# Kernel tuning notes

Measured on AMD Instinct MI355X. Metric: run time of the kernel, lower is better.

Reference implementation:

```python
import math
import jax, jax.numpy as jnp
import numpy as np

MAX_T = 300
B, T, V, D, H = 16, 256, 25, 128, 8


def _layernorm(x, g, b):
    m = x.mean(-1, keepdims=True)
    var = ((x - m) ** 2).mean(-1, keepdims=True)
    return (x - m) / jnp.sqrt(var + 1e-5) * g + b


def setup_inputs() -> dict:
    key = jax.random.key(0)
    ks = jax.random.split(key, 8)
    d = D // H
    init = lambda k, shape: jax.random.normal(k, shape, dtype=jnp.float32) * 0.02
    return dict(
        x=jax.random.normal(ks[0], (B, T, V, D), dtype=jnp.float32),
        ln1_g=jnp.ones((D,), jnp.float32), ln1_b=jnp.zeros((D,), jnp.float32),
        qkv_w=init(ks[1], (D, 3 * D)), qkv_b=jnp.zeros((3 * D,), jnp.float32),
        proj_w=init(ks[2], (D, D)), proj_b=jnp.zeros((D,), jnp.float32),
        logit_scale=jnp.full((H, 1, 1), math.log(math.sqrt(d)), dtype=jnp.float32),
        rel_pos_bias=init(ks[3], (H, 2 * MAX_T - 1)),
        ln2_g=jnp.ones((D,), jnp.float32), ln2_b=jnp.zeros((D,), jnp.float32),
        ffn_w1=init(ks[4], (D, 4 * D)), ffn_b1=jnp.zeros((4 * D,), jnp.float32),
        ffn_w2=init(ks[5], (4 * D, D)), ffn_b2=jnp.zeros((D,), jnp.float32),
    )


def reference(x, ln1_g, ln1_b, qkv_w, qkv_b, proj_w, proj_b, logit_scale,
              rel_pos_bias, ln2_g, ln2_b, ffn_w1, ffn_b1, ffn_w2, ffn_b2):
    b, t, v_, dm = x.shape
    h = logit_scale.shape[0]
    d = dm // h
    # (B, T, V, D) -> (B*V, T, D): attention runs over frames per joint
    xf = x.transpose(0, 2, 1, 3).reshape(b * v_, t, dm)
    res = xf
    xn = _layernorm(xf, ln1_g, ln1_b)
    qkv = (xn @ qkv_w + qkv_b).reshape(b * v_, t, 3, h, d).transpose(2, 0, 3, 1, 4)
    q, k, v = qkv[0], qkv[1], qkv[2]  # (BV, h, T, d)
    scale = jnp.exp(jnp.minimum(logit_scale, math.log(100.0)))  # (h,1,1)
    qn = q / jnp.maximum(jnp.linalg.norm(q, axis=-1, keepdims=True), 1e-12) * scale
    kn = k / jnp.maximum(jnp.linalg.norm(k, axis=-1, keepdims=True), 1e-12)
    # learned relative-position bias, gathered to (h, T, T)
    coords = jnp.arange(t)
    rel = coords[:, None] - coords[None, :] + (MAX_T - 1)
    bias = rel_pos_bias[:, rel]
    # SDPA applies its default 1/sqrt(head_dim) scale on top of logit_scale
    scores = jnp.einsum('bhtd,bhsd->bhts', qn, kn) / math.sqrt(d) + bias[None]
    attn = jax.nn.softmax(scores, axis=-1)
    out = jnp.einsum('bhts,bhsd->bhtd', attn, v)
    out = out.transpose(0, 2, 1, 3).reshape(b * v_, t, dm)
    xf = res + (out @ proj_w + proj_b)
    y = _layernorm(xf, ln2_g, ln2_b)
    y = jax.nn.gelu(y @ ffn_w1 + ffn_b1, approximate=False) @ ffn_w2 + ffn_b2
    xf = xf + y
    return xf.reshape(b, v_, t, dm).transpose(0, 2, 1, 3)
```

## Files before the change

### kernel.cpp

```cpp
#include <hip/hip_runtime.h>
#include <hip/hip_fp16.h>
#include <math.h>

#define B_   16
#define T_   256
#define V_   25
#define D_   128
#define H_   8
#define DH   16
#define BV_  (B_*V_)
#define MAXT 300
#define NREL (2*MAXT-1)

typedef __attribute__((ext_vector_type(8))) short short8;
typedef __attribute__((ext_vector_type(4))) float f32x4;
typedef __attribute__((ext_vector_type(4))) _Float16 half4;
typedef __attribute__((ext_vector_type(8))) _Float16 half8;

__device__ inline short f2bf(float f) {
  union { float f; unsigned u; } a; a.f = f;
  unsigned r = (a.u + 0x7FFF + ((a.u >> 16) & 1)) >> 16;
  return (short)r;
}

__device__ inline float gelu_fast(float u) {
  float s = u * fmaf(0.0713548162726f, u*u, 1.5957691216057f);
  return u * __builtin_amdgcn_rcpf(1.0f + __expf(-s));
}

__global__ __launch_bounds__(256) void k0_prep(
    const float* __restrict__ qkv_w, const float* __restrict__ pw,
    const float* __restrict__ w1,    const float* __restrict__ w2,
    short* __restrict__ qkv_wt, short* __restrict__ pwt,
    _Float16* __restrict__ w1t, _Float16* __restrict__ w2t)
{
  int i = blockIdx.x*256 + threadIdx.x;
  if (i < 384*128) { int n = i >> 7, k = i & 127; qkv_wt[i] = f2bf(qkv_w[k*384 + n]); }
  if (i < 128*128) { int n = i >> 7, k = i & 127; pwt[i]    = f2bf(pw[k*128 + n]); }
  if (i < 512*128) { int n = i >> 7, k = i & 127; w1t[i]    = (_Float16)w1[k*512 + n]; }
  if (i < 128*512) {
    int r = i & 3, lane = (i >> 2) & 63, hn = (i >> 8) & 31, ot = i >> 13;
    int k = hn*16 + (lane >> 4)*4 + r;
    int n = ot*16 + (lane & 15);
    w2t[i] = (_Float16)w2[k*128 + n];
  }
}

__global__ __launch_bounds__(256) void k1_ln_qkv(
    const float* __restrict__ x, const float* __restrict__ g1, const float* __restrict__ b1,
    const short* __restrict__ qkv_wt, const float* __restrict__ qkv_b,
    const float* __restrict__ logit_scale,
    _Float16* __restrict__ qb, _Float16* __restrict__ kb, _Float16* __restrict__ vt)
{
  __shared__ short xn[64][136];
  const int tid = threadIdx.x;
  const int bv  = blockIdx.x / (T_/64);
  const int t0  = (blockIdx.x % (T_/64)) * 64;
  const int b   = bv / V_, v = bv % V_;

  {
    const int j = tid & 15;
    float4 gA = *(const float4*)(g1 + j*8), gB = *(const float4*)(g1 + j*8 + 4);
    float4 bA = *(const float4*)(b1 + j*8), bB = *(const float4*)(b1 + j*8 + 4);
    float gg[8] = {gA.x,gA.y,gA.z,gA.w,gB.x,gB.y,gB.z,gB.w};
    float bb[8] = {bA.x,bA.y,bA.z,bA.w,bB.x,bB.y,bB.z,bB.w};
    for (int rep = 0; rep < 4; ++rep) {
      const int tok = rep*16 + (tid >> 4);
      const float* xp = x + (((size_t)b*T_ + (t0+tok))*V_ + v)*D_ + j*8;
      float4 a0 = *(const float4*)xp;
      float4 a1 = *(const float4*)(xp+4);
      float e[8] = {a0.x,a0.y,a0.z,a0.w,a1.x,a1.y,a1.z,a1.w};
      float s = 0.f;
      #pragma unroll
      for (int q = 0; q < 8; ++q) s += e[q];
      #pragma unroll
      for (int m = 1; m < 16; m <<= 1) s += __shfl_xor(s, m, 16);
      float mean = s * (1.0f/128.0f);
      float s2 = 0.f;
      #pragma unroll
      for (int q = 0; q < 8; ++q) { float d = e[q]-mean; s2 += d*d; }
      #pragma unroll
      for (int m = 1; m < 16; m <<= 1) s2 += __shfl_xor(s2, m, 16);
      float rstd = rsqrtf(s2*(1.0f/128.0f) + 1e-5f);
      short8 o;
      #pragma unroll
      for (int q = 0; q < 8; ++q) o[q] = f2bf((e[q]-mean)*rstd*gg[q] + bb[q]);
      *(short8*)&xn[tok][j*8] = o;
    }
  }
  __syncthreads();

  const int wave = tid >> 6, lane = tid & 63;
  const int col = lane & 15, quad = lane >> 4;
  short8 af[4][4];
  #pragma unroll
  for (int tt = 0; tt < 4; ++tt)
    #pragma unroll
    for (int kk = 0; kk < 4; ++kk)
      af[tt][kk] = *(const short8*)&xn[tt*16+col][kk*32 + quad*8];

  for (int it = 0; it < 6; ++it) {
    const int tile = wave*6 + it;
    const int n0 = tile*16;
    short8 bf[4];
    #pragma unroll
    for (int kk = 0; kk < 4; ++kk)
      bf[kk] = *(const short8*)(qkv_wt + (size_t)(n0+col)*128 + kk*32 + quad*8);
    f32x4 acc[4] = {{0.f,0.f,0.f,0.f},{0.f,0.f,0.f,0.f},{0.f,0.f,0.f,0.f},{0.f,0.f,0.f,0.f}};
    #pragma unroll
    for (int kk = 0; kk < 4; ++kk)
      #pragma unroll
      for (int tt = 0; tt < 4; ++tt)
        acc[tt] = __builtin_amdgcn_mfma_f32_16x16x32_bf16(af[tt][kk], bf[kk], acc[tt], 0, 0, 0);
    const float bias = qkv_b[n0+col];
    const int h = tile & 7;
    const size_t bh = (size_t)bv*H_ + h;
    if (tile < 16) {
      const float scale = (tile < 8)
        ? __expf(fminf(logit_scale[h], 4.605170185988091f)) * 0.25f : 1.0f;
      #pragma unroll
      for (int tt = 0; tt < 4; ++tt) {
        float val[4], inv[4];
        #pragma unroll
        for (int r = 0; r < 4; ++r) {
          val[r] = acc[tt][r] + bias;
          float s = val[r]*val[r];
          #pragma unroll
          for (int m = 1; m < 16; m <<= 1) s += __shfl_xor(s, m, 16);
          inv[r] = 1.0f / fmaxf(sqrtf(s), 1e-12f);
        }
        const size_t obase = (bh*T_ + (t0 + tt*16 + quad*4))*DH + col;
        if (tile < 8) {
          #pragma unroll
          for (int r = 0; r < 4; ++r) qb[obase + (size_t)r*DH] = (_Float16)(val[r]*inv[r]*scale);
        } else {
          #pragma unroll
          for (int r = 0; r < 4; ++r) kb[obase + (size_t)r*DH] = (_Float16)(val[r]*inv[r]);
        }
      }
    } else {
      #pragma unroll
      for (int tt = 0; tt < 4; ++tt) {
        half4 vh;
        #pragma unroll
        for (int r = 0; r < 4; ++r) vh[r] = (_Float16)(acc[tt][r] + bias);
        *(half4*)(vt + bh*4096 + (size_t)(t0/16 + tt)*256 + col*16 + quad*4) = vh;
      }
    }
  }
}

__global__ __launch_bounds__(256) void k2_attn(
    const float* __restrict__ rel_pos_bias,
    const _Float16* __restrict__ qb, const _Float16* __restrict__ kb,
    const _Float16* __restrict__ vt, float* __restrict__ xattn)
{
  __shared__ float bias_s[NREL + 1];
  const int tid = threadIdx.x;
  const int bh  = blockIdx.x;
  const int h   = bh & (H_-1);
  const int bv  = bh >> 3;
  for (int j = tid; j < NREL; j += 256) bias_s[j] = rel_pos_bias[h*NREL + j];
  __syncthreads();

  const int wave = tid >> 6, lane = tid & 63;
  const int nn = lane & 15, quad = lane >> 4;
  const size_t qkbase = (size_t)bh * (T_*DH);
  const size_t vbase  = (size_t)bh * 4096;

  half4 qf[4];
  #pragma unroll
  for (int tt = 0; tt < 4; ++tt)
    qf[tt] = *(const half4*)(qb + qkbase + (size_t)(wave*64 + tt*16 + nn)*DH + quad*4);

  f32x4 o[4];
  #pragma unroll
  for (int tt = 0; tt < 4; ++tt) o[tt] = (f32x4){0.f,0.f,0.f,0.f};
  float lsum[4] = {0.f,0.f,0.f,0.f};

  half4 kf = *(const half4*)(kb + qkbase + (size_t)nn*DH + quad*4);
  half4 vf = *(const half4*)(vt + vbase + (size_t)nn*16 + quad*4);

  for (int s16 = 0; s16 < 16; ++s16) {
    half4 kf_n, vf_n;
    if (s16 < 15) {
      kf_n = *(const half4*)(kb + qkbase + (size_t)((s16+1)*16 + nn)*DH + quad*4);
      vf_n = *(const half4*)(vt + vbase + (size_t)(s16+1)*256 + nn*16 + quad*4);
    }
    #pragma unroll
    for (int tt = 0; tt < 4; ++tt) {
      f32x4 c = {0.f,0.f,0.f,0.f};
      c = __builtin_amdgcn_mfma_f32_16x16x16f16(kf, qf[tt], c, 0, 0, 0);
      const int ib = (wave*64 + tt*16 + nn) - (s16*16 + quad*4) + (MAXT-1);
      half4 pa;
      #pragma unroll
      for (int r = 0; r < 4; ++r) {
        float p = __expf(c[r] + bias_s[ib - r]);
        lsum[tt] += p;
        pa[r] = (_Float16)p;
      }
      o[tt] = __builtin_amdgcn_mfma_f32_16x16x16f16(pa, vf, o[tt], 0, 0, 0);
    }
    kf = kf_n; vf = vf_n;
  }

  #pragma unroll
  for (int tt = 0; tt < 4; ++tt) {
    float l = lsum[tt];
    l += __shfl_xor(l, 16);
    l += __shfl_xor(l, 32);
    float rinv = 1.0f / l;
    #pragma unroll
    for (int r = 0; r < 4; ++r) {
      float inv = __shfl(rinv, quad*4 + r, 16);
      const int t = wave*64 + tt*16 + quad*4 + r;
      xattn[((size_t)bv*T_ + t)*D_ + h*DH + nn] = o[tt][r] * inv;
    }
  }
}

__global__ __launch_bounds__(256) void k3_proj(
    const float* __restrict__ x, const short* __restrict__ pwt,
    const float* __restrict__ proj_b, float* __restrict__ xf2)
{
  __shared__ short a_s[64][136];
  const int tid = threadIdx.x;
  const int bv  = blockIdx.x / (T_/64);
  const int t0  = (blockIdx.x % (T_/64)) * 64;
  const int b   = bv / V_, v = bv % V_;

  {
    const int j = tid & 15;
    for (int rep = 0; rep < 4; ++rep) {
      const int tok = rep*16 + (tid >> 4);
      const float* ap = xf2 + ((size_t)bv*T_ + t0+tok)*D_ + j*8;
      float4 a0 = *(const float4*)ap;
      float4 a1 = *(const float4*)(ap+4);
      float e[8] = {a0.x,a0.y,a0.z,a0.w,a1.x,a1.y,a1.z,a1.w};
      short8 o;
      #pragma unroll
      for (int q = 0; q < 8; ++q) o[q] = f2bf(e[q]);
      *(short8*)&a_s[tok][j*8] = o;
    }
  }
  __syncthreads();

  const int wave = tid >> 6, lane = tid & 63;
  const int col = lane & 15, quad = lane >> 4;
  short8 af[4][4];
  #pragma unroll
  for (int tt = 0; tt < 4; ++tt)
    #pragma unroll
    for (int kk = 0; kk < 4; ++kk)
      af[tt][kk] = *(const short8*)&a_s[tt*16+col][kk*32 + quad*8];

  for (int it = 0; it < 2; ++it) {
    const int n0 = (wave*2 + it)*16;
    short8 bf[4];
    #pragma unroll
    for (int kk = 0; kk < 4; ++kk)
      bf[kk] = *(const short8*)(pwt + (size_t)(n0+col)*128 + kk*32 + quad*8);
    f32x4 acc[4] = {{0.f,0.f,0.f,0.f},{0.f,0.f,0.f,0.f},{0.f,0.f,0.f,0.f},{0.f,0.f,0.f,0.f}};
    #pragma unroll
    for (int kk = 0; kk < 4; ++kk)
      #pragma unroll
      for (int tt = 0; tt < 4; ++tt)
        acc[tt] = __builtin_amdgcn_mfma_f32_16x16x32_bf16(af[tt][kk], bf[kk], acc[tt], 0, 0, 0);
    const float pbv = proj_b[n0+col];
    #pragma unroll
    for (int tt = 0; tt < 4; ++tt)
      #pragma unroll
      for (int r = 0; r < 4; ++r) {
        const int t = t0 + tt*16 + quad*4 + r;
        float res = x[(((size_t)b*T_ + t)*V_ + v)*D_ + n0 + col];
        xf2[((size_t)bv*T_ + t)*D_ + n0 + col] = acc[tt][r] + pbv + res;
      }
  }
}

__global__ __launch_bounds__(256) void k4_ffn(
    const float* __restrict__ xf2, const float* __restrict__ g2, const float* __restrict__ b2,
    const _Float16* __restrict__ w1t, const float* __restrict__ fb1,
    const _Float16* __restrict__ w2t, const float* __restrict__ fb2,
    float* __restrict__ out)
{
  __shared__ _Float16 y_s[128][136];
  __shared__ _Float16 w1c[64][136];
  __shared__ _Float16 w2c[8192];
  const int tid = threadIdx.x;
  const int bv  = blockIdx.x / (T_/128);
  const int t0  = (blockIdx.x % (T_/128)) * 128;
  const int b   = bv / V_, v = bv % V_;

  {
    const int j = tid & 15;
    float4 gA = *(const float4*)(g2 + j*8), gB = *(const float4*)(g2 + j*8 + 4);
    float4 bA = *(const float4*)(b2 + j*8), bB = *(const float4*)(b2 + j*8 + 4);
    float gg[8] = {gA.x,gA.y,gA.z,gA.w,gB.x,gB.y,gB.z,gB.w};
    float bb[8] = {bA.x,bA.y,bA.z,bA.w,bB.x,bB.y,bB.z,bB.w};
    for (int rep = 0; rep < 8; ++rep) {
      const int tok = rep*16 + (tid >> 4);
      const float* xp = xf2 + ((size_t)bv*T_ + t0+tok)*D_ + j*8;
      float4 a0 = *(const float4*)xp;
      float4 a1 = *(const float4*)(xp+4);
      float e[8] = {a0.x,a0.y,a0.z,a0.w,a1.x,a1.y,a1.z,a1.w};
      float s = 0.f;
      #pragma unroll
      for (int q = 0; q < 8; ++q) s += e[q];
      #pragma unroll
      for (int m = 1; m < 16; m <<= 1) s += __shfl_xor(s, m, 16);
      float mean = s * (1.0f/128.0f);
      float s2 = 0.f;
      #pragma unroll
      for (int q = 0; q < 8; ++q) { float d = e[q]-mean; s2 += d*d; }
      #pragma unroll
      for (int m = 1; m < 16; m <<= 1) s2 += __shfl_xor(s2, m, 16);
      float rstd = rsqrtf(s2*(1.0f/128.0f) + 1e-5f);
      half8 o;
      #pragma unroll
      for (int q = 0; q < 8; ++q) o[q] = (_Float16)((e[q]-mean)*rstd*gg[q] + bb[q]);
      *(half8*)&y_s[tok][j*8] = o;
    }
  }
  __syncthreads();

  const int wave = tid >> 6, lane = tid & 63;
  const int col = lane & 15, quad = lane >> 4;

  half8 yf[2][4];
  #pragma unroll
  for (int tt = 0; tt < 2; ++tt)
    #pragma unroll
    for (int kk = 0; kk < 4; ++kk)
      yf[tt][kk] = *(const half8*)&y_s[wave*32 + tt*16 + col][kk*32 + quad*8];

  f32x4 acc2[2][8];
  #pragma unroll
  for (int tt = 0; tt < 2; ++tt)
    #pragma unroll
    for (int ot = 0; ot < 8; ++ot) acc2[tt][ot] = (f32x4){0.f,0.f,0.f,0.f};

  for (int c = 0; c < 8; ++c) {
    __syncthreads();
    #pragma unroll
    for (int j = 0; j < 4; ++j) {
      const int u = j*256 + tid;
      const int row = u >> 4, seg = u & 15;
      *(half8*)&w1c[row][seg*8] = *(const half8*)(w1t + (size_t)(c*64+row)*128 + seg*8);
    }
    #pragma unroll
    for (int j = 0; j < 4; ++j) {
      const int u = j*256 + tid;
      const int off16 = u & 31, hk = (u >> 5) & 3, ot = u >> 7;
      *(half8*)&w2c[(size_t)u*8] =
        *(const half8*)(w2t + ((size_t)(ot*32 + c*4 + hk)*64)*4 + off16*8);
    }
    __syncthreads();

    #pragma unroll
    for (int ht = 0; ht < 4; ++ht) {
      half8 w1f[4];
      #pragma unroll
      for (int kk = 0; kk < 4; ++kk)
        w1f[kk] = *(const half8*)&w1c[ht*16+col][kk*32 + quad*8];
      f32x4 c0 = {0.f,0.f,0.f,0.f}, c1 = {0.f,0.f,0.f,0.f};
      #pragma unroll
      for (int kk = 0; kk < 4; ++kk) {
        c0 = __builtin_amdgcn_mfma_f32_16x16x32_f16(w1f[kk], yf[0][kk], c0, 0, 0, 0);
        c1 = __builtin_amdgcn_mfma_f32_16x16x32_f16(w1f[kk], yf[1][kk], c1, 0, 0, 0);
      }
      const int hn = c*4 + ht;
      const f32x4 b1v = *(const f32x4*)(fb1 + hn*16 + quad*4);
      half4 pa0, pa1;
      #pragma unroll
      for (int r = 0; r < 4; ++r) {
        pa0[r] = (_Float16)gelu_fast(c0[r] + b1v[r]);
        pa1[r] = (_Float16)gelu_fast(c1[r] + b1v[r]);
      }
      #pragma unroll
      for (int ot = 0; ot < 8; ++ot) {
        half4 w2f = *(const half4*)&w2c[((ot*4 + ht)*64 + lane)*4];
        acc2[0][ot] = __builtin_amdgcn_mfma_f32_16x16x16f16(pa0, w2f, acc2[0][ot], 0, 0, 0);
        acc2[1][ot] = __builtin_amdgcn_mfma_f32_16x16x16f16(pa1, w2f, acc2[1][ot], 0, 0, 0);
      }
    }
  }

  const int tw = t0 + wave*32;
  #pragma unroll
  for (int tt = 0; tt < 2; ++tt)
    #pragma unroll
    for (int ot = 0; ot < 8; ++ot) {
      const float bo = fb2[ot*16 + col];
      #pragma unroll
      for (int r = 0; r < 4; ++r) {
        const int t = tw + tt*16 + quad*4 + r;
        float val = acc2[tt][ot][r] + bo + xf2[((size_t)bv*T_ + t)*D_ + ot*16 + col];
        out[(((size_t)b*T_ + t)*V_ + v)*D_ + ot*16 + col] = val;
      }
    }
}

extern "C" void kernel_launch(void* const* d_in, const int* in_sizes, int n_in,
                              void* d_out, int out_size, void* d_ws, size_t ws_size,
                              hipStream_t stream)
{
  (void)in_sizes; (void)n_in; (void)out_size; (void)ws_size;
  const float* x     = (const float*)d_in[0];
  const float* g1    = (const float*)d_in[1];
  const float* b1    = (const float*)d_in[2];
  const float* qkv_w = (const float*)d_in[3];
  const float* qkv_b = (const float*)d_in[4];
  const float* pw    = (const float*)d_in[5];
  const float* pb    = (const float*)d_in[6];
  const float* ls    = (const float*)d_in[7];
  const float* rpb   = (const float*)d_in[8];
  const float* g2    = (const float*)d_in[9];
  const float* b2    = (const float*)d_in[10];
  const float* w1    = (const float*)d_in[11];
  const float* fb1   = (const float*)d_in[12];
  const float* w2    = (const float*)d_in[13];
  const float* fb2   = (const float*)d_in[14];
  float* out = (float*)d_out;

  const size_t n = (size_t)BV_*T_*D_;
  char* ws = (char*)d_ws;
  _Float16* qb  = (_Float16*)ws;
  _Float16* kb  = (_Float16*)(ws + n*2);
  float*    xf2 = (float*)(ws + n*4);
  _Float16* vt  = (_Float16*)(ws + n*8);
  short*    qkv_wt = (short*)(ws + n*10);
  short*    pwt    = qkv_wt + 384*128;
  _Float16* w1t    = (_Float16*)(pwt + 128*128);
  _Float16* w2t    = w1t + 512*128;

  k0_prep  <<<256,          dim3(256), 0, stream>>>(qkv_w, pw, w1, w2, qkv_wt, pwt, w1t, w2t);
  k1_ln_qkv<<<BV_*(T_/64),  dim3(256), 0, stream>>>(x, g1, b1, qkv_wt, qkv_b, ls, qb, kb, vt);
  k2_attn  <<<BV_*H_,       dim3(256), 0, stream>>>(rpb, qb, kb, vt, xf2);
  k3_proj  <<<BV_*(T_/64),  dim3(256), 0, stream>>>(x, pwt, pb, xf2);
  k4_ffn   <<<BV_*(T_/128), dim3(256), 0, stream>>>(xf2, g2, b2, w1t, fb1, w2t, fb2, out);
}
```

Baseline: 346.8 us.

## Read FFN weights directly from global memory instead of staging in LDS

The FFN kernel no longer stages W1 and W2 chunks through shared memory with barriers. Each wave now loads its MFMA weight fragments straight from global memory (through L1/L2), which removes about 33 KB of LDS per block and 16 block-wide syncs. Launch bounds are raised to ask for 4 blocks per CU so occupancy can go up. The cost is redundant global/L2 traffic, since all four waves in a block load the same weights, and possible register pressure under the tighter launch bound.

```diff
diff --git a/kernel.cpp b/kernel.cpp
--- a/kernel.cpp
+++ b/kernel.cpp
@@ -278,15 +278,13 @@
   }
 }
 
-__global__ __launch_bounds__(256) void k4_ffn(
+__global__ __launch_bounds__(256, 4) void k4_ffn(
     const float* __restrict__ xf2, const float* __restrict__ g2, const float* __restrict__ b2,
     const _Float16* __restrict__ w1t, const float* __restrict__ fb1,
     const _Float16* __restrict__ w2t, const float* __restrict__ fb2,
     float* __restrict__ out)
 {
   __shared__ _Float16 y_s[128][136];
-  __shared__ _Float16 w1c[64][136];
-  __shared__ _Float16 w2c[8192];
   const int tid = threadIdx.x;
   const int bv  = blockIdx.x / (T_/128);
   const int t0  = (blockIdx.x % (T_/128)) * 128;
@@ -340,49 +338,26 @@
     #pragma unroll
     for (int ot = 0; ot < 8; ++ot) acc2[tt][ot] = (f32x4){0.f,0.f,0.f,0.f};
 
-  for (int c = 0; c < 8; ++c) {
-    __syncthreads();
-    #pragma unroll
-    for (int j = 0; j < 4; ++j) {
-      const int u = j*256 + tid;
-      const int row = u >> 4, seg = u & 15;
-      *(half8*)&w1c[row][seg*8] = *(const half8*)(w1t + (size_t)(c*64+row)*128 + seg*8);
-    }
-    #pragma unroll
-    for (int j = 0; j < 4; ++j) {
-      const int u = j*256 + tid;
-      const int off16 = u & 31, hk = (u >> 5) & 3, ot = u >> 7;
-      *(half8*)&w2c[(size_t)u*8] =
-        *(const half8*)(w2t + ((size_t)(ot*32 + c*4 + hk)*64)*4 + off16*8);
-    }
-    __syncthreads();
-
-    #pragma unroll
-    for (int ht = 0; ht < 4; ++ht) {
-      half8 w1f[4];
-      #pragma unroll
-      for (int kk = 0; kk < 4; ++kk)
-        w1f[kk] = *(const half8*)&w1c[ht*16+col][kk*32 + quad*8];
-      f32x4 c0 = {0.f,0.f,0.f,0.f}, c1 = {0.f,0.f,0.f,0.f};
-      #pragma unroll
-      for (int kk = 0; kk < 4; ++kk) {
-        c0 = __builtin_amdgcn_mfma_f32_16x16x32_f16(w1f[kk], yf[0][kk], c0, 0, 0, 0);
-        c1 = __builtin_amdgcn_mfma_f32_16x16x32_f16(w1f[kk], yf[1][kk], c1, 0, 0, 0);
-      }
-      const int hn = c*4 + ht;
-      const f32x4 b1v = *(const f32x4*)(fb1 + hn*16 + quad*4);
-      half4 pa0, pa1;
-      #pragma unroll
-      for (int r = 0; r < 4; ++r) {
-        pa0[r] = (_Float16)gelu_fast(c0[r] + b1v[r]);
-        pa1[r] = (_Float16)gelu_fast(c1[r] + b1v[r]);
-      }
-      #pragma unroll
-      for (int ot = 0; ot < 8; ++ot) {
-        half4 w2f = *(const half4*)&w2c[((ot*4 + ht)*64 + lane)*4];
-        acc2[0][ot] = __builtin_amdgcn_mfma_f32_16x16x16f16(pa0, w2f, acc2[0][ot], 0, 0, 0);
-        acc2[1][ot] = __builtin_amdgcn_mfma_f32_16x16x16f16(pa1, w2f, acc2[1][ot], 0, 0, 0);
-      }
+  for (int hn = 0; hn < 32; ++hn) {
+    f32x4 c0 = {0.f,0.f,0.f,0.f}, c1 = {0.f,0.f,0.f,0.f};
+    #pragma unroll
+    for (int kk = 0; kk < 4; ++kk) {
+      half8 w1f = *(const half8*)(w1t + (size_t)(hn*16+col)*128 + kk*32 + quad*8);
+      c0 = __builtin_amdgcn_mfma_f32_16x16x32_f16(w1f, yf[0][kk], c0, 0, 0, 0);
+      c1 = __builtin_amdgcn_mfma_f32_16x16x32_f16(w1f, yf[1][kk], c1, 0, 0, 0);
+    }
+    const f32x4 b1v = *(const f32x4*)(fb1 + hn*16 + quad*4);
+    half4 pa0, pa1;
+    #pragma unroll
+    for (int r = 0; r < 4; ++r) {
+      pa0[r] = (_Float16)gelu_fast(c0[r] + b1v[r]);
+      pa1[r] = (_Float16)gelu_fast(c1[r] + b1v[r]);
+    }
+    #pragma unroll
+    for (int ot = 0; ot < 8; ++ot) {
+      half4 w2f = *(const half4*)(w2t + ((size_t)(ot*32 + hn)*64 + lane)*4);
+      acc2[0][ot] = __builtin_amdgcn_mfma_f32_16x16x16f16(pa0, w2f, acc2[0][ot], 0, 0, 0);
+      acc2[1][ot] = __builtin_amdgcn_mfma_f32_16x16x16f16(pa1, w2f, acc2[1][ot], 0, 0, 0);
     }
   }
 
```

Result: slower. 357.6 us (+3.1%).

## Double-buffer FFN weight chunks and use wider K=32 MFMA for second GEMM

Applied to the files above, without the earlier changes.

Rewrites the FFN kernel to prefetch each weight chunk into registers while computing the previous chunk from a second shared-memory buffer, with the first buffer aliased onto the LayerNorm staging area. The w2 layout is repacked so the second GEMM can use 16x16x32 f16 MFMAs over pairs of hidden tiles instead of 16x16x16. The LayerNorm row loads are also software-pipelined. The goal is to hide global load latency and issue fewer MFMA instructions, at the cost of more registers and a larger shared-memory footprint, which may reduce occupancy.

```diff
diff --git a/kernel.cpp b/kernel.cpp
--- a/kernel.cpp
+++ b/kernel.cpp
@@ -39,8 +39,8 @@
   if (i < 128*128) { int n = i >> 7, k = i & 127; pwt[i]    = f2bf(pw[k*128 + n]); }
   if (i < 512*128) { int n = i >> 7, k = i & 127; w1t[i]    = (_Float16)w1[k*512 + n]; }
   if (i < 128*512) {
-    int r = i & 3, lane = (i >> 2) & 63, hn = (i >> 8) & 31, ot = i >> 13;
-    int k = hn*16 + (lane >> 4)*4 + r;
+    int e = i & 7, lane = (i >> 3) & 63, hp = (i >> 9) & 15, ot = i >> 13;
+    int k = hp*32 + ((e >> 2) << 4) + ((lane >> 4) << 2) + (e & 3);
     int n = ot*16 + (lane & 15);
     w2t[i] = (_Float16)w2[k*128 + n];
   }
@@ -284,25 +284,53 @@
     const _Float16* __restrict__ w2t, const float* __restrict__ fb2,
     float* __restrict__ out)
 {
-  __shared__ _Float16 y_s[128][136];
-  __shared__ _Float16 w1c[64][136];
-  __shared__ _Float16 w2c[8192];
+  __shared__ __align__(16) char smem[68608];
+  _Float16 (*y_s)[136]  = (_Float16 (*)[136])smem;
+  _Float16 (*w1cB)[136] = (_Float16 (*)[136])smem;
+  _Float16 *w2cB        = (_Float16*)(smem + 17408);
+  _Float16 (*w1cA)[136] = (_Float16 (*)[136])(smem + 34816);
+  _Float16 *w2cA        = (_Float16*)(smem + 34816 + 17408);
+
   const int tid = threadIdx.x;
   const int bv  = blockIdx.x / (T_/128);
   const int t0  = (blockIdx.x % (T_/128)) * 128;
   const int b   = bv / V_, v = bv % V_;
 
+  half8 p_w1[4], p_w2[4];
+  auto STAGE_ISSUE = [&](int c) {
+    #pragma unroll
+    for (int j = 0; j < 4; ++j) {
+      const int u = j*256 + tid;
+      p_w1[j] = *(const half8*)(w1t + (size_t)(c*64 + (u >> 4))*128 + (u & 15)*8);
+      p_w2[j] = *(const half8*)(w2t + (size_t)(((u >> 7)*16 + c*2 + ((u >> 6) & 1))*64 + (u & 63))*8);
+    }
+  };
+  auto COMMIT = [&](_Float16 (*w1d)[136], _Float16* w2d) {
+    #pragma unroll
+    for (int j = 0; j < 4; ++j) {
+      const int u = j*256 + tid;
+      *(half8*)&w1d[u >> 4][(u & 15)*8] = p_w1[j];
+      *(half8*)&w2d[(size_t)u*8]        = p_w2[j];
+    }
+  };
+
+  STAGE_ISSUE(0);
+
   {
-    const int j = tid & 15;
+    const int j = tid & 15, trow = tid >> 4;
     float4 gA = *(const float4*)(g2 + j*8), gB = *(const float4*)(g2 + j*8 + 4);
     float4 bA = *(const float4*)(b2 + j*8), bB = *(const float4*)(b2 + j*8 + 4);
     float gg[8] = {gA.x,gA.y,gA.z,gA.w,gB.x,gB.y,gB.z,gB.w};
     float bb[8] = {bA.x,bA.y,bA.z,bA.w,bB.x,bB.y,bB.z,bB.w};
+    const float* xp = xf2 + ((size_t)bv*T_ + t0 + trow)*D_ + j*8;
+    float4 a0 = *(const float4*)xp;
+    float4 a1 = *(const float4*)(xp+4);
     for (int rep = 0; rep < 8; ++rep) {
-      const int tok = rep*16 + (tid >> 4);
-      const float* xp = xf2 + ((size_t)bv*T_ + t0+tok)*D_ + j*8;
-      float4 a0 = *(const float4*)xp;
-      float4 a1 = *(const float4*)(xp+4);
+      float4 n0, n1;
+      if (rep < 7) {
+        const float* np = xp + (size_t)(rep+1)*16*D_;
+        n0 = *(const float4*)np; n1 = *(const float4*)(np+4);
+      }
       float e[8] = {a0.x,a0.y,a0.z,a0.w,a1.x,a1.y,a1.z,a1.w};
       float s = 0.f;
       #pragma unroll
@@ -319,9 +347,13 @@
       half8 o;
       #pragma unroll
       for (int q = 0; q < 8; ++q) o[q] = (_Float16)((e[q]-mean)*rstd*gg[q] + bb[q]);
-      *(half8*)&y_s[tok][j*8] = o;
-    }
-  }
+      *(half8*)&y_s[rep*16 + trow][j*8] = o;
+      a0 = n0; a1 = n1;
+    }
+  }
+
+  COMMIT(w1cA, w2cA);
+  STAGE_ISSUE(1);
   __syncthreads();
 
   const int wave = tid >> 6, lane = tid & 63;
@@ -333,6 +365,7 @@
     #pragma unroll
     for (int kk = 0; kk < 4; ++kk)
       yf[tt][kk] = *(const half8*)&y_s[wave*32 + tt*16 + col][kk*32 + quad*8];
+  __syncthreads();
 
   f32x4 acc2[2][8];
   #pragma unroll
@@ -340,50 +373,51 @@
     #pragma unroll
     for (int ot = 0; ot < 8; ++ot) acc2[tt][ot] = (f32x4){0.f,0.f,0.f,0.f};
 
-  for (int c = 0; c < 8; ++c) {
+  auto COMPUTE = [&](int c, _Float16 (*w1s)[136], const _Float16* w2s) {
+    #pragma unroll
+    for (int hpl = 0; hpl < 2; ++hpl) {
+      const int htL = hpl*2, htH = hpl*2 + 1;
+      f32x4 cl0 = {0.f,0.f,0.f,0.f}, cl1 = {0.f,0.f,0.f,0.f};
+      f32x4 ch0 = {0.f,0.f,0.f,0.f}, ch1 = {0.f,0.f,0.f,0.f};
+      #pragma unroll
+      for (int kk = 0; kk < 4; ++kk) {
+        half8 wl = *(const half8*)&w1s[htL*16+col][kk*32 + quad*8];
+        half8 wh = *(const half8*)&w1s[htH*16+col][kk*32 + quad*8];
+        cl0 = __builtin_amdgcn_mfma_f32_16x16x32_f16(wl, yf[0][kk], cl0, 0, 0, 0);
+        cl1 = __builtin_amdgcn_mfma_f32_16x16x32_f16(wl, yf[1][kk], cl1, 0, 0, 0);
+        ch0 = __builtin_amdgcn_mfma_f32_16x16x32_f16(wh, yf[0][kk], ch0, 0, 0, 0);
+        ch1 = __builtin_amdgcn_mfma_f32_16x16x32_f16(wh, yf[1][kk], ch1, 0, 0, 0);
+      }
+      const f32x4 bL = *(const f32x4*)(fb1 + (c*4 + htL)*16 + quad*4);
+      const f32x4 bH = *(const f32x4*)(fb1 + (c*4 + htH)*16 + quad*4);
+      half8 pa0, pa1;
+      #pragma unroll
+      for (int r = 0; r < 4; ++r) {
+        pa0[r]   = (_Float16)gelu_fast(cl0[r] + bL[r]);
+        pa0[4+r] = (_Float16)gelu_fast(ch0[r] + bH[r]);
+        pa1[r]   = (_Float16)gelu_fast(cl1[r] + bL[r]);
+        pa1[4+r] = (_Float16)gelu_fast(ch1[r] + bH[r]);
+      }
+      #pragma unroll
+      for (int ot = 0; ot < 8; ++ot) {
+        half8 w2f = *(const half8*)&w2s[((ot*2 + hpl)*64 + lane)*8];
+        acc2[0][ot] = __builtin_amdgcn_mfma_f32_16x16x32_f16(pa0, w2f, acc2[0][ot], 0, 0, 0);
+        acc2[1][ot] = __builtin_amdgcn_mfma_f32_16x16x32_f16(pa1, w2f, acc2[1][ot], 0, 0, 0);
+      }
+    }
+  };
+
+  for (int cc = 0; cc < 8; cc += 2) {
+    COMMIT(w1cB, w2cB);
+    if (cc + 2 < 8) STAGE_ISSUE(cc + 2);
+    COMPUTE(cc, w1cA, w2cA);
     __syncthreads();
-    #pragma unroll
-    for (int j = 0; j < 4; ++j) {
-      const int u = j*256 + tid;
-      const int row = u >> 4, seg = u & 15;
-      *(half8*)&w1c[row][seg*8] = *(const half8*)(w1t + (size_t)(c*64+row)*128 + seg*8);
-    }
-    #pragma unroll
-    for (int j = 0; j < 4; ++j) {
-      const int u = j*256 + tid;
-      const int off16 = u & 31, hk = (u >> 5) & 3, ot = u >> 7;
-      *(half8*)&w2c[(size_t)u*8] =
-        *(const half8*)(w2t + ((size_t)(ot*32 + c*4 + hk)*64)*4 + off16*8);
-    }
+    if (cc + 2 < 8) {
+      COMMIT(w1cA, w2cA);
+      STAGE_ISSUE(cc + 3);
+    }
+    COMPUTE(cc + 1, w1cB, w2cB);
     __syncthreads();
-
-    #pragma unroll
-    for (int ht = 0; ht < 4; ++ht) {
-      half8 w1f[4];
-      #pragma unroll
-      for (int kk = 0; kk < 4; ++kk)
-        w1f[kk] = *(const half8*)&w1c[ht*16+col][kk*32 + quad*8];
-      f32x4 c0 = {0.f,0.f,0.f,0.f}, c1 = {0.f,0.f,0.f,0.f};
-      #pragma unroll
-      for (int kk = 0; kk < 4; ++kk) {
-        c0 = __builtin_amdgcn_mfma_f32_16x16x32_f16(w1f[kk], yf[0][kk], c0, 0, 0, 0);
-        c1 = __builtin_amdgcn_mfma_f32_16x16x32_f16(w1f[kk], yf[1][kk], c1, 0, 0, 0);
-      }
-      const int hn = c*4 + ht;
-      const f32x4 b1v = *(const f32x4*)(fb1 + hn*16 + quad*4);
-      half4 pa0, pa1;
-      #pragma unroll
-      for (int r = 0; r < 4; ++r) {
-        pa0[r] = (_Float16)gelu_fast(c0[r] + b1v[r]);
-        pa1[r] = (_Float16)gelu_fast(c1[r] + b1v[r]);
-      }
-      #pragma unroll
-      for (int ot = 0; ot < 8; ++ot) {
-        half4 w2f = *(const half4*)&w2c[((ot*4 + ht)*64 + lane)*4];
-        acc2[0][ot] = __builtin_amdgcn_mfma_f32_16x16x16f16(pa0, w2f, acc2[0][ot], 0, 0, 0);
-        acc2[1][ot] = __builtin_amdgcn_mfma_f32_16x16x16f16(pa1, w2f, acc2[1][ot], 0, 0, 0);
-      }
-    }
   }
 
   const int tw = t0 + wave*32;
```

Measured after the change: 344.3 us. No clear change (-0.7%).
